# Optimization experiments

Hardware: AMD Instinct MI355X
Metric: run time of the kernel (lower is better)

Reference implementation:

```python
import jax, jax.numpy as jnp
import numpy as np

N_DRUG, N_CELL, N_GENE = 2048, 2048, 4096
N = N_DRUG + N_CELL + N_GENE
E = 262144
H1, H2, H3, HEADS = 256, 64, 64, 4
N_PAIRS = 10000
EPS = 1e-5


def _gatv2(x, src, dst, Wl, bl, Wr, br, att, bias, heads, out_ch):
    # PyG GATv2Conv: e_ij = att . leaky_relu(Wl x_j + Wr x_i), softmax over incoming edges of i,
    # out_i = sum_j alpha_ij * (Wl x_j), heads concatenated, plus output bias.
    n = x.shape[0]
    xl = (x @ Wl + bl).reshape(n, heads, out_ch)   # source transform
    xr = (x @ Wr + br).reshape(n, heads, out_ch)   # target transform
    e = jax.nn.leaky_relu(xl[src] + xr[dst], 0.2)  # [E, H, C]
    logits = jnp.einsum('ehc,hc->eh', e, att)      # [E, H]
    m = jax.ops.segment_max(logits, dst, num_segments=n)
    ex = jnp.exp(logits - m[dst])
    denom = jax.ops.segment_sum(ex, dst, num_segments=n)
    alpha = ex / denom[dst]                        # [E, H]
    out = jax.ops.segment_sum(xl[src] * alpha[:, :, None], dst, num_segments=n)
    return out.reshape(n, heads * out_ch) + bias, alpha


def _graph_norm(x, gamma, beta, mscale):
    # PyG GraphNorm over a single graph: out = (x - a*mean) / sqrt(var + eps) * gamma + beta
    mu = x.mean(0)
    sub = x - mu * mscale
    var = (sub * sub).mean(0)
    return sub / jnp.sqrt(var + EPS) * gamma + beta


def setup_inputs() -> dict:
    key = jax.random.key(0)
    ks = jax.random.split(key, 24)
    f = jnp.float32
    nrm = lambda k, shape, sc: jax.random.normal(k, shape, f) * sc
    drug = jax.random.normal(ks[0], (N_DRUG, N_DRUG), f)
    cell = jax.random.normal(ks[1], (N_CELL, N_CELL), f)
    gene = jax.random.normal(ks[2], (N_GENE, N_GENE), f)
    # random edges guaranteed to have no self loops (PyG would remove then re-add them)
    src = jax.random.randint(ks[3], (E,), 0, N)
    off = jax.random.randint(ks[4], (E,), 1, N)
    edges = jnp.stack([src, (src + off) % N]).astype(jnp.int32)
    idx_drug = jax.random.randint(ks[5], (N_PAIRS,), 0, N_DRUG)
    idx_cell = N_DRUG + jax.random.randint(ks[6], (N_PAIRS,), 0, N_CELL)
    HC2, HC3 = HEADS * H2, HEADS * H3
    return {
        'drug': drug, 'cell': cell, 'gene': gene,
        'edges': edges, 'idx_drug': idx_drug, 'idx_cell': idx_cell,
        'W_drug': nrm(ks[7], (N_DRUG, H1), 1 / np.sqrt(N_DRUG)), 'b_drug': jnp.zeros((H1,), f),
        'W_cell': nrm(ks[8], (N_CELL, H1), 1 / np.sqrt(N_CELL)), 'b_cell': jnp.zeros((H1,), f),
        'W_gene': nrm(ks[9], (N_GENE, H1), 1 / np.sqrt(N_GENE)), 'b_gene': jnp.zeros((H1,), f),
        'gat1_Wl': nrm(ks[10], (H1, HC2), 1 / np.sqrt(H1)), 'gat1_bl': jnp.zeros((HC2,), f),
        'gat1_Wr': nrm(ks[11], (H1, HC2), 1 / np.sqrt(H1)), 'gat1_br': jnp.zeros((HC2,), f),
        'gat1_att': nrm(ks[12], (HEADS, H2), 1 / np.sqrt(H2)), 'gat1_bias': jnp.zeros((HC2,), f),
        'gat2_Wl': nrm(ks[13], (HC2, HC3), 1 / np.sqrt(HC2)), 'gat2_bl': jnp.zeros((HC3,), f),
        'gat2_Wr': nrm(ks[14], (HC2, HC3), 1 / np.sqrt(HC2)), 'gat2_br': jnp.zeros((HC3,), f),
        'gat2_att': nrm(ks[15], (HEADS, H3), 1 / np.sqrt(H3)), 'gat2_bias': jnp.zeros((HC3,), f),
        'gn1_gamma': jnp.ones((HC2,), f), 'gn1_beta': jnp.zeros((HC2,), f), 'gn1_scale': jnp.ones((HC2,), f),
        'gn2_gamma': jnp.ones((HC3,), f), 'gn2_beta': jnp.zeros((HC3,), f), 'gn2_scale': jnp.ones((HC3,), f),
        'lin1_W': nrm(ks[16], (2 * HC3, 1), 1 / np.sqrt(2 * HC3)), 'lin1_b': jnp.zeros((1,), f),
    }


def reference(drug, cell, gene, edges, idx_drug, idx_cell,
              W_drug, b_drug, W_cell, b_cell, W_gene, b_gene,
              gat1_Wl, gat1_bl, gat1_Wr, gat1_br, gat1_att, gat1_bias,
              gat2_Wl, gat2_bl, gat2_Wr, gat2_br, gat2_att, gat2_bias,
              gn1_gamma, gn1_beta, gn1_scale, gn2_gamma, gn2_beta, gn2_scale,
              lin1_W, lin1_b):
    x = jnp.concatenate([drug @ W_drug + b_drug,
                         cell @ W_cell + b_cell,
                         gene @ W_gene + b_gene], axis=0)  # [N, H1]
    loops = jnp.arange(N, dtype=edges.dtype)
    src = jnp.concatenate([edges[0], loops])  # GATv2Conv adds self loops
    dst = jnp.concatenate([edges[1], loops])
    x, a1 = _gatv2(x, src, dst, gat1_Wl, gat1_bl, gat1_Wr, gat1_br, gat1_att, gat1_bias, HEADS, H2)
    x = jax.nn.relu(_graph_norm(x, gn1_gamma, gn1_beta, gn1_scale))  # dropout = identity (eval)
    x, a2 = _gatv2(x, src, dst, gat2_Wl, gat2_bl, gat2_Wr, gat2_br, gat2_att, gat2_bias, HEADS, H3)
    x = jax.nn.relu(_graph_norm(x, gn2_gamma, gn2_beta, gn2_scale))
    pair = jnp.concatenate([x[idx_drug], x[idx_cell]], axis=1)  # [P, 2*H*H3]
    pred = jax.nn.sigmoid(pair @ lin1_W + lin1_b)
    # get_attention_mat: dense [N,N], every edge position set to the (detached) scalar mean of
    # attention weights; the two layer matrices share edge positions so they simply add.
    val = jax.lax.stop_gradient(a1.mean() + a2.mean())
    attn = jnp.zeros((N, N), x.dtype).at[src, dst].set(val)
    return pred, attn
```

## Files before the change

### kernel.cpp

```cpp
#include <hip/hip_runtime.h>

#define NNODES 8192
#define NEDGE  262144
#define EETOT  270336
#define NPAIRS 10000

typedef __attribute__((ext_vector_type(8))) short s16x8;
typedef __attribute__((ext_vector_type(8))) unsigned short u16x8;
typedef __attribute__((ext_vector_type(4))) float f32x4;

__device__ __forceinline__ float lrelu(float v) { return v > 0.f ? v : 0.2f * v; }

__device__ __forceinline__ void split2(float a, unsigned short& h, unsigned short& l) {
  unsigned u = __float_as_uint(a);
  h = (unsigned short)(u >> 16);
  float hf = __uint_as_float(u & 0xffff0000u);
  float r = a - hf;
  unsigned v = __float_as_uint(r);
  v += 0x7fffu + ((v >> 16) & 1u);
  l = (unsigned short)(v >> 16);
}

__device__ __forceinline__ unsigned short f2bf(float f) {
  unsigned u = __float_as_uint(f);
  u += 0x7fffu + ((u >> 16) & 1u);
  return (unsigned short)(u >> 16);
}
__device__ __forceinline__ float bf2f(unsigned short u) {
  return __uint_as_float((unsigned)u << 16);
}

__device__ __forceinline__ void wsplit_body(const float* __restrict__ W,
    unsigned short* __restrict__ Th, int K, int blk) {
  int col = threadIdx.x;
  int kb = blk * 8;
  u16x8 vh;
#pragma unroll
  for (int i = 0; i < 8; ++i)
    vh[i] = f2bf(W[(size_t)(kb + i) * 256 + col]);
  *(u16x8*)(Th + (size_t)col * K + kb) = vh;
}

__global__ __launch_bounds__(256) void k_wsplit_all(
    const float* __restrict__ Wd, const float* __restrict__ Wc, const float* __restrict__ Wg,
    const float* __restrict__ W1l, const float* __restrict__ W1r,
    const float* __restrict__ W2l, const float* __restrict__ W2r,
    unsigned short* __restrict__ tdh, unsigned short* __restrict__ tch,
    unsigned short* __restrict__ tgh,
    unsigned short* __restrict__ tl1h, unsigned short* __restrict__ tr1h,
    unsigned short* __restrict__ tl2h, unsigned short* __restrict__ tr2h,
    int* __restrict__ counts_d, int* __restrict__ counts_s, float* __restrict__ stats) {
  int b = blockIdx.x;
  if      (b < 256)  wsplit_body(Wd,  tdh, 2048, b);
  else if (b < 512)  wsplit_body(Wc,  tch, 2048, b - 256);
  else if (b < 1024) wsplit_body(Wg,  tgh, 4096, b - 512);
  else if (b < 1056) { wsplit_body(W1l, tl1h, 256, b - 1024);
                       counts_d[(b - 1024) * 256 + threadIdx.x] = 0; }
  else if (b < 1088) { wsplit_body(W1r, tr1h, 256, b - 1056);
                       counts_s[(b - 1056) * 256 + threadIdx.x] = 0; }
  else if (b < 1120) { wsplit_body(W2l, tl2h, 256, b - 1088);
                       if (b < 1092) stats[(b - 1088) * 256 + threadIdx.x] = 0.f; }
  else               wsplit_body(W2r, tr2h, 256, b - 1120);
}

struct Tile128 {
  unsigned short Ah[128][40], Al[128][40], Bh[128][40];
};
struct TileN {
  Tile128 t;
  float nsc[256], nsh[256];
};

template<bool BIAS, bool OUTBF, bool NORM>
__device__ __forceinline__ void gemm_tile128(Tile128& s,
    const float* __restrict__ A, int lda,
    const unsigned short* __restrict__ Th, int ldb, int nsteps,
    const float* __restrict__ bias, float* __restrict__ C,
    unsigned short* __restrict__ Cb,
    const float* __restrict__ nsc, const float* __restrict__ nsh) {
  const int tid = threadIdx.x;
  const int wave = tid >> 6, lane = tid & 63;
  const int g = lane >> 4, r = lane & 15;
  const int wr = (wave >> 1) * 64, wc = (wave & 1) * 64;

  const int ar = tid >> 1, ak = (tid & 1) * 16;
  const float* Arow = A + (size_t)ar * lda + ak;
  const int bc = tid & 127, bk = (tid >> 7) * 16;
  const unsigned short* Bhs = Th + (size_t)bc * ldb + bk;

  f32x4 acc[4][4];
#pragma unroll
  for (int m = 0; m < 4; ++m)
#pragma unroll
    for (int n = 0; n < 4; ++n)
#pragma unroll
      for (int j = 0; j < 4; ++j) acc[m][n][j] = 0.f;

  float4 qa0 = *(const float4*)(Arow);
  float4 qa1 = *(const float4*)(Arow + 4);
  float4 qa2 = *(const float4*)(Arow + 8);
  float4 qa3 = *(const float4*)(Arow + 12);
  u16x8 qb0 = *(const u16x8*)(Bhs);
  u16x8 qb1 = *(const u16x8*)(Bhs + 8);
  float4 pa0, pa1, pa2, pa3;
  u16x8 pb0, pb1;
  if (nsteps > 1) {
    pa0 = *(const float4*)(Arow + 32);
    pa1 = *(const float4*)(Arow + 36);
    pa2 = *(const float4*)(Arow + 40);
    pa3 = *(const float4*)(Arow + 44);
    pb0 = *(const u16x8*)(Bhs + 32);
    pb1 = *(const u16x8*)(Bhs + 40);
  }

  for (int t = 0; t < nsteps; ++t) {
    {
      float av[16] = {qa0.x, qa0.y, qa0.z, qa0.w, qa1.x, qa1.y, qa1.z, qa1.w,
                      qa2.x, qa2.y, qa2.z, qa2.w, qa3.x, qa3.y, qa3.z, qa3.w};
      u16x8 vh0, vh1, vl0, vl1;
#pragma unroll
      for (int i = 0; i < 16; ++i) {
        float v = av[i];
        if constexpr (NORM) {
          int ch = t * 32 + ak + i;
          v = fmaxf(v * nsc[ch] + nsh[ch], 0.f);
        }
        unsigned short hh, ll;
        split2(v, hh, ll);
        if (i < 8) { vh0[i] = hh; vl0[i] = ll; }
        else       { vh1[i - 8] = hh; vl1[i - 8] = ll; }
      }
      *(u16x8*)&s.Ah[ar][ak]     = vh0;
      *(u16x8*)&s.Ah[ar][ak + 8] = vh1;
      *(u16x8*)&s.Al[ar][ak]     = vl0;
      *(u16x8*)&s.Al[ar][ak + 8] = vl1;
      *(u16x8*)&s.Bh[bc][bk]     = qb0;
      *(u16x8*)&s.Bh[bc][bk + 8] = qb1;
    }
    __syncthreads();
    qa0 = pa0; qa1 = pa1; qa2 = pa2; qa3 = pa3;
    qb0 = pb0; qb1 = pb1;
    if (t + 2 < nsteps) {
      const float* An = Arow + (size_t)(t + 2) * 32;
      pa0 = *(const float4*)(An);
      pa1 = *(const float4*)(An + 4);
      pa2 = *(const float4*)(An + 8);
      pa3 = *(const float4*)(An + 12);
      const unsigned short* Bhn = Bhs + (size_t)(t + 2) * 32;
      pb0 = *(const u16x8*)(Bhn);
      pb1 = *(const u16x8*)(Bhn + 8);
    }
    s16x8 fah[4], fal[4], fbh[4];
#pragma unroll
    for (int m = 0; m < 4; ++m) {
      fah[m] = *(const s16x8*)&s.Ah[wr + m * 16 + r][g * 8];
      fal[m] = *(const s16x8*)&s.Al[wr + m * 16 + r][g * 8];
    }
#pragma unroll
    for (int n = 0; n < 4; ++n)
      fbh[n] = *(const s16x8*)&s.Bh[wc + n * 16 + r][g * 8];
#pragma unroll
    for (int m = 0; m < 4; ++m)
#pragma unroll
      for (int n = 0; n < 4; ++n) {
        acc[m][n] = __builtin_amdgcn_mfma_f32_16x16x32_bf16(fal[m], fbh[n], acc[m][n], 0, 0, 0);
        acc[m][n] = __builtin_amdgcn_mfma_f32_16x16x32_bf16(fah[m], fbh[n], acc[m][n], 0, 0, 0);
      }
    __syncthreads();
  }
#pragma unroll
  for (int m = 0; m < 4; ++m)
#pragma unroll
    for (int n = 0; n < 4; ++n) {
      int col = wc + n * 16 + r;
      float bv = BIAS ? bias[col] : 0.f;
      int rowb = wr + m * 16 + g * 4;
#pragma unroll
      for (int j = 0; j < 4; ++j) {
        float v = acc[m][n][j] + bv;
        if constexpr (OUTBF) Cb[(size_t)(rowb + j) * 256 + col] = f2bf(v);
        else                 C[(size_t)(rowb + j) * 256 + col] = v;
      }
    }
}

#define PDRUG_PLANE ((size_t)2048 * 256)
#define PGENE_PLANE ((size_t)4096 * 256)
__global__ __launch_bounds__(256) void k_inproj_fill(
    const float* __restrict__ drug, const float* __restrict__ cell,
    const float* __restrict__ gene,
    const unsigned short* __restrict__ tdh, const unsigned short* __restrict__ tch,
    const unsigned short* __restrict__ tgh, float* __restrict__ P,
    const int* __restrict__ csrdst, const int* __restrict__ rowst_s,
    float* __restrict__ attn) {
  __shared__ Tile128 s;
  int b = blockIdx.x;
  if (b >= 512) {
    int row = b - 512;
    float* rp = attn + (size_t)row * NNODES;
    f32x4* p4 = (f32x4*)rp;
    f32x4 z = {0.f, 0.f, 0.f, 0.f};
#pragma unroll
    for (int j = 0; j < 8; ++j)
      __builtin_nontemporal_store(z, p4 + j * 256 + threadIdx.x);
    __syncthreads();
    int e0 = rowst_s[row], e1 = rowst_s[row + 1];
    for (int j = e0 + (int)threadIdx.x; j < e1; j += 256)
      rp[csrdst[j]] = 16384.0f / 270336.0f;
    return;
  }
  if (b < 256) {
    int idx = b & 127;
    int colblk = (idx >> 3) & 1;
    int rest = (idx & 7) | ((idx >> 4) << 3);
    int rowblk = rest >> 2, chunk = rest & 3;
    const float* X = (b < 128) ? drug : cell;
    const unsigned short* Th = (b < 128) ? tdh : tch;
    float* Pb = P + ((b < 128) ? 0 : 4 * PDRUG_PLANE);
    gemm_tile128<false, false, false>(s,
        X + (size_t)rowblk * 128 * 2048 + (size_t)chunk * 512, 2048,
        Th + (size_t)colblk * 128 * 2048 + chunk * 512, 2048, 16, nullptr,
        Pb + (size_t)chunk * PDRUG_PLANE + (size_t)rowblk * 128 * 256 + colblk * 128,
        nullptr, nullptr, nullptr);
  } else {
    int idx = b - 256;
    int colblk = (idx >> 3) & 1;
    int rest = (idx & 7) | ((idx >> 4) << 3);
    int rowblk = rest >> 2, chunk = rest & 3;
    gemm_tile128<false, false, false>(s,
        gene + (size_t)rowblk * 128 * 4096 + (size_t)chunk * 1024, 4096,
        tgh + (size_t)colblk * 128 * 4096 + chunk * 1024, 4096, 32, nullptr,
        P + 8 * PDRUG_PLANE + (size_t)chunk * PGENE_PLANE + (size_t)rowblk * 128 * 256 + colblk * 128,
        nullptr, nullptr, nullptr);
  }
}

__global__ __launch_bounds__(256) void k_reduce(const float* __restrict__ P,
    const float* __restrict__ bd, const float* __restrict__ bc,
    const float* __restrict__ bg, float* __restrict__ out) {
  int idx = blockIdx.x * 256 + threadIdx.x;
  size_t e = (size_t)idx * 4;
  int row = (int)(e >> 8);
  int col = (int)(e & 255);
  const float* base; const float* bias; size_t plane;
  if (row < 2048) {
    base = P + (size_t)row * 256 + col; bias = bd; plane = PDRUG_PLANE;
  } else if (row < 4096) {
    base = P + 4 * PDRUG_PLANE + (size_t)(row - 2048) * 256 + col; bias = bc;
    plane = PDRUG_PLANE;
  } else {
    base = P + 8 * PDRUG_PLANE + (size_t)(row - 4096) * 256 + col; bias = bg;
    plane = PGENE_PLANE;
  }
  float4 s = *(const float4*)(base);
#pragma unroll
  for (int p = 1; p < 4; ++p) {
    float4 v = *(const float4*)(base + p * plane);
    s.x += v.x; s.y += v.y; s.z += v.z; s.w += v.w;
  }
  float4 bv = *(const float4*)(bias + col);
  s.x += bv.x; s.y += bv.y; s.z += bv.z; s.w += bv.w;
  *(float4*)(out + e) = s;
}

template<bool NORM>
__global__ __launch_bounds__(256) void k_gemm2(const float* __restrict__ A,
    const unsigned short* __restrict__ ThL, const unsigned short* __restrict__ ThR,
    const float* __restrict__ biasL, const float* __restrict__ biasR,
    unsigned short* __restrict__ CLb, unsigned short* __restrict__ CRb,
    const float* __restrict__ csum, const float* __restrict__ csumsq,
    const float* __restrict__ gamma, const float* __restrict__ beta,
    const float* __restrict__ mscale) {
  __shared__ TileN s;
  int b = blockIdx.x;
  int sub = (b >> 3) & 3;
  int x = (b & 7) | ((b >> 5) << 3);
  if constexpr (NORM) {
    int c = threadIdx.x;
    float mu = csum[c] * (1.0f / 8192.0f);
    float ex2 = csumsq[c] * (1.0f / 8192.0f);
    float smu = mscale[c] * mu;
    float var = ex2 - 2.f * smu * mu + smu * smu;
    float sc = rsqrtf(var + 1e-5f) * gamma[c];
    s.nsc[c] = sc;
    s.nsh[c] = beta[c] - smu * sc;
    __syncthreads();
  }
  int row0 = x * 128;
  int col0 = (sub & 1) * 128;
  if (sub >= 2) {
    gemm_tile128<true, true, NORM>(s.t, A + (size_t)row0 * 256, 256,
        ThR + (size_t)col0 * 256, 256, 8,
        biasR + col0, nullptr, CRb + (size_t)row0 * 256 + col0, s.nsc, s.nsh);
  } else {
    gemm_tile128<true, true, NORM>(s.t, A + (size_t)row0 * 256, 256,
        ThL + (size_t)col0 * 256, 256, 8,
        biasL + col0, nullptr, CLb + (size_t)row0 * 256 + col0, s.nsc, s.nsh);
  }
}

__global__ void k_count2(const int* __restrict__ edges, int* __restrict__ cd,
                         int* __restrict__ cs) {
  int e = blockIdx.x * blockDim.x + threadIdx.x;
  if (e >= EETOT) return;
  int s, d;
  if (e < NEDGE) { s = edges[e]; d = edges[NEDGE + e]; } else { s = d = e - NEDGE; }
  atomicAdd(&cd[d], 1);
  atomicAdd(&cs[s], 1);
}

__global__ __launch_bounds__(1024) void k_scan2(
    const int* __restrict__ c0, int* __restrict__ r0, int* __restrict__ u0,
    const int* __restrict__ c1, int* __restrict__ r1, int* __restrict__ u1) {
  const int* counts = blockIdx.x ? c1 : c0;
  int* row_start = blockIdx.x ? r1 : r0;
  int* cursor = blockIdx.x ? u1 : u0;
  __shared__ int part[1024];
  int t = threadIdx.x;
  int base = t * 8;
  int loc[8];
  int s = 0;
#pragma unroll
  for (int j = 0; j < 8; ++j) { loc[j] = s; s += counts[base + j]; }
  part[t] = s;
  __syncthreads();
  for (int off = 1; off < 1024; off <<= 1) {
    int v = (t >= off) ? part[t - off] : 0;
    __syncthreads();
    part[t] += v;
    __syncthreads();
  }
  int pre = (t == 0) ? 0 : part[t - 1];
#pragma unroll
  for (int j = 0; j < 8; ++j) {
    int v = pre + loc[j];
    row_start[base + j] = v;
    cursor[base + j] = v;
  }
  if (t == 1023) row_start[NNODES] = pre + s;
}

__global__ void k_place2(const int* __restrict__ edges, int* __restrict__ curd,
    int* __restrict__ curs, int* __restrict__ csrsrc, int* __restrict__ csrdst) {
  int e = blockIdx.x * blockDim.x + threadIdx.x;
  if (e >= EETOT) return;
  int s, d;
  if (e < NEDGE) { s = edges[e]; d = edges[NEDGE + e]; } else { s = d = e - NEDGE; }
  int pd = atomicAdd(&curd[d], 1);
  csrsrc[pd] = s;
  int ps = atomicAdd(&curs[s], 1);
  csrdst[ps] = d;
}

__global__ __launch_bounds__(256) void k_gat(
    const unsigned short* __restrict__ xl, const unsigned short* __restrict__ xr,
    const float* __restrict__ att, const int* __restrict__ csrsrc,
    const int* __restrict__ row_start, const float* __restrict__ bias,
    float* __restrict__ out) {
  int i = blockIdx.x * 4 + (threadIdx.x >> 6);
  int lane = threadIdx.x & 63;
  int co = (lane >> 4) * 64 + (lane & 15) * 4;
  float4 w4 = *(const float4*)(att + co);
  ushort4 ur = *(const ushort4*)(xr + (size_t)i * 256 + co);
  float4 r4;
  r4.x = bf2f(ur.x); r4.y = bf2f(ur.y); r4.z = bf2f(ur.z); r4.w = bf2f(ur.w);
  float sum = 0.f, ax = 0.f, ay = 0.f, az = 0.f, aw = 0.f;
  int e0 = row_start[i], e1 = row_start[i + 1];
  int deg = e1 - e0;

  for (int cb = 0; cb < deg; cb += 64) {
    int cn = min(deg - cb, 64);
    int myid = (lane < cn) ? csrsrc[e0 + cb + lane] : 0;
    auto g = [&](int j) {
      int s = __shfl(myid, j);
      return *(const ushort4*)(xl + (size_t)s * 256 + co);
    };
    ushort4 cur[8], nxt[8];
    int curn = min(cn, 8);
#pragma unroll
    for (int j = 0; j < 8; ++j)
      if (j < curn) cur[j] = g(j);
    int p = curn;
    for (;;) {
      int nxtn = min(cn - p, 8);
#pragma unroll
      for (int j = 0; j < 8; ++j)
        if (j < nxtn) nxt[j] = g(p + j);
#pragma unroll
      for (int j = 0; j < 8; ++j) {
        if (j >= curn) break;
        ushort4 u = cur[j];
        float x0 = bf2f(u.x), x1 = bf2f(u.y), x2 = bf2f(u.z), x3 = bf2f(u.w);
        float t = w4.x * lrelu(x0 + r4.x) + w4.y * lrelu(x1 + r4.y) +
                  w4.z * lrelu(x2 + r4.z) + w4.w * lrelu(x3 + r4.w);
        t += __shfl_xor(t, 1);
        t += __shfl_xor(t, 2);
        t += __shfl_xor(t, 4);
        t += __shfl_xor(t, 8);
        float el = __expf(fminf(t, 60.f));
        sum += el;
        ax += el * x0; ay += el * x1; az += el * x2; aw += el * x3;
      }
      if (nxtn <= 0) break;
#pragma unroll
      for (int j = 0; j < 8; ++j) cur[j] = nxt[j];
      curn = nxtn; p += nxtn;
    }
  }
  float inv = 1.0f / sum;
  float4 bv = *(const float4*)(bias + co);
  float4 r;
  r.x = ax * inv + bv.x; r.y = ay * inv + bv.y;
  r.z = az * inv + bv.z; r.w = aw * inv + bv.w;
  *(float4*)(out + (size_t)i * 256 + co) = r;
}

__global__ __launch_bounds__(256) void k_colstats(const float* __restrict__ x,
    float* __restrict__ csum, float* __restrict__ csumsq) {
  int c = threadIdx.x;
  int r0 = blockIdx.x * 32;
  float s = 0.f, s2 = 0.f;
  for (int r = 0; r < 32; ++r) {
    float v = x[(size_t)(r0 + r) * 256 + c];
    s += v; s2 += v * v;
  }
  atomicAdd(&csum[c], s);
  atomicAdd(&csumsq[c], s2);
}

__global__ __launch_bounds__(256) void k_pred(const float* __restrict__ h,
    const int* __restrict__ idx_drug, const int* __restrict__ idx_cell,
    const float* __restrict__ W, const float* __restrict__ b,
    const float* __restrict__ csum, const float* __restrict__ csumsq,
    const float* __restrict__ gamma, const float* __restrict__ beta,
    const float* __restrict__ mscale, float* __restrict__ out) {
  int p = blockIdx.x * 4 + (threadIdx.x >> 6);
  if (p >= NPAIRS) return;
  int lane = threadIdx.x & 63;
  int rd = idx_drug[p], rc = idx_cell[p];
  float4 a  = *(const float4*)(h + (size_t)rd * 256 + lane * 4);
  float4 cg = *(const float4*)(h + (size_t)rc * 256 + lane * 4);
  float4 wa = *(const float4*)(W + lane * 4);
  float4 wc = *(const float4*)(W + 256 + lane * 4);
  float av[4] = {a.x, a.y, a.z, a.w};
  float cv[4] = {cg.x, cg.y, cg.z, cg.w};
  float wv[4] = {wa.x, wa.y, wa.z, wa.w};
  float uv[4] = {wc.x, wc.y, wc.z, wc.w};
  float t = 0.f;
#pragma unroll
  for (int j = 0; j < 4; ++j) {
    int ch = lane * 4 + j;
    float mu = csum[ch] * (1.0f / 8192.0f);
    float ex2 = csumsq[ch] * (1.0f / 8192.0f);
    float smu = mscale[ch] * mu;
    float var = ex2 - 2.f * smu * mu + smu * smu;
    float sc = rsqrtf(var + 1e-5f) * gamma[ch];
    float sh = beta[ch] - smu * sc;
    t += fmaxf(av[j] * sc + sh, 0.f) * wv[j] + fmaxf(cv[j] * sc + sh, 0.f) * uv[j];
  }
#pragma unroll
  for (int off = 1; off < 64; off <<= 1) t += __shfl_xor(t, off);
  if (lane == 0) out[p] = 1.0f / (1.0f + __expf(-(t + b[0])));
}

extern "C" void kernel_launch(void* const* d_in, const int* in_sizes, int n_in,
                              void* d_out, int out_size, void* d_ws, size_t ws_size,
                              hipStream_t stream) {
  const float* drug = (const float*)d_in[0];
  const float* cell = (const float*)d_in[1];
  const float* gene = (const float*)d_in[2];
  const int*   edges = (const int*)d_in[3];
  const int*   idxd = (const int*)d_in[4];
  const int*   idxc = (const int*)d_in[5];
  const float* Wd = (const float*)d_in[6];   const float* bd = (const float*)d_in[7];
  const float* Wc = (const float*)d_in[8];   const float* bc = (const float*)d_in[9];
  const float* Wg = (const float*)d_in[10];  const float* bg = (const float*)d_in[11];
  const float* g1Wl = (const float*)d_in[12]; const float* g1bl = (const float*)d_in[13];
  const float* g1Wr = (const float*)d_in[14]; const float* g1br = (const float*)d_in[15];
  const float* g1att = (const float*)d_in[16]; const float* g1bias = (const float*)d_in[17];
  const float* g2Wl = (const float*)d_in[18]; const float* g2bl = (const float*)d_in[19];
  const float* g2Wr = (const float*)d_in[20]; const float* g2br = (const float*)d_in[21];
  const float* g2att = (const float*)d_in[22]; const float* g2bias = (const float*)d_in[23];
  const float* gn1g = (const float*)d_in[24]; const float* gn1b = (const float*)d_in[25];
  const float* gn1s = (const float*)d_in[26];
  const float* gn2g = (const float*)d_in[27]; const float* gn2b = (const float*)d_in[28];
  const float* gn2s = (const float*)d_in[29];
  const float* linW = (const float*)d_in[30]; const float* linb = (const float*)d_in[31];
  float* out = (float*)d_out;
  (void)in_sizes; (void)n_in; (void)out_size; (void)ws_size;

  char* ws = (char*)d_ws;
  size_t off = 0;
  auto take = [&](size_t bytes) -> void* {
    void* p = ws + off;
    off += (bytes + 255) & ~(size_t)255;
    return p;
  };
  float* bufA = (float*)take((size_t)NNODES * 256 * 4);
  unsigned short* bufBb = (unsigned short*)take((size_t)NNODES * 256 * 2);
  unsigned short* bufCb = (unsigned short*)take((size_t)NNODES * 256 * 2);
  int* counts_d = (int*)take((size_t)NNODES * 4);
  int* counts_s = (int*)take((size_t)NNODES * 4);
  float* stats  = (float*)take(4 * 256 * 4);
  int* rowst_d  = (int*)take((size_t)(NNODES + 1) * 4);
  int* rowst_s  = (int*)take((size_t)(NNODES + 1) * 4);
  int* cursor_d = (int*)take((size_t)NNODES * 4);
  int* cursor_s = (int*)take((size_t)NNODES * 4);
  int* csrsrc   = (int*)take((size_t)EETOT * 4);
  int* csrdst   = (int*)take((size_t)EETOT * 4);
  unsigned short* tdh = (unsigned short*)take((size_t)256 * 2048 * 2);
  unsigned short* tch = (unsigned short*)take((size_t)256 * 2048 * 2);
  unsigned short* tgh = (unsigned short*)take((size_t)256 * 4096 * 2);
  unsigned short* tl1h = (unsigned short*)take((size_t)256 * 256 * 2);
  unsigned short* tr1h = (unsigned short*)take((size_t)256 * 256 * 2);
  unsigned short* tl2h = (unsigned short*)take((size_t)256 * 256 * 2);
  unsigned short* tr2h = (unsigned short*)take((size_t)256 * 256 * 2);
  float* Ppart = (float*)take((8 * PDRUG_PLANE + 4 * PGENE_PLANE) * 4);

  k_wsplit_all<<<1152, 256, 0, stream>>>(Wd, Wc, Wg, g1Wl, g1Wr, g2Wl, g2Wr,
      tdh, tch, tgh, tl1h, tr1h, tl2h, tr2h, counts_d, counts_s, stats);

  k_count2<<<EETOT / 256, 256, 0, stream>>>(edges, counts_d, counts_s);
  k_scan2<<<2, 1024, 0, stream>>>(counts_d, rowst_d, cursor_d, counts_s, rowst_s, cursor_s);
  k_place2<<<EETOT / 256, 256, 0, stream>>>(edges, cursor_d, cursor_s, csrsrc, csrdst);

  k_inproj_fill<<<512 + NNODES, 256, 0, stream>>>(drug, cell, gene, tdh, tch, tgh,
      Ppart, csrdst, rowst_s, out + NPAIRS);
  k_reduce<<<NNODES * 256 / 4 / 256, 256, 0, stream>>>(Ppart, bd, bc, bg, bufA);

  k_gemm2<false><<<256, 256, 0, stream>>>(bufA, tl1h, tr1h, g1bl, g1br,
      bufBb, bufCb, nullptr, nullptr, nullptr, nullptr, nullptr);
  k_gat<<<NNODES / 4, 256, 0, stream>>>(bufBb, bufCb, g1att, csrsrc, rowst_d, g1bias, bufA);
  k_colstats<<<NNODES / 32, 256, 0, stream>>>(bufA, stats, stats + 256);

  k_gemm2<true><<<256, 256, 0, stream>>>(bufA, tl2h, tr2h, g2bl, g2br,
      bufBb, bufCb, stats, stats + 256, gn1g, gn1b, gn1s);
  k_gat<<<NNODES / 4, 256, 0, stream>>>(bufBb, bufCb, g2att, csrsrc, rowst_d, g2bias, bufA);
  k_colstats<<<NNODES / 32, 256, 0, stream>>>(bufA, stats + 512, stats + 768);

  k_pred<<<NPAIRS / 4, 256, 0, stream>>>(bufA, idxd, idxc, linW, linb,
      stats + 512, stats + 768, gn2g, gn2b, gn2s, out);
}
```

Before: 291.1 us.

## Spread dense attention-matrix fill across GEMM and GAT kernels

The 8192x8192 attention matrix fill (zeroing plus edge scatter) used to run entirely as extra blocks of the input-projection kernel. It is now split into 1024-row slices appended as extra blocks to the input projection, both small GEMMs and both GAT kernels. The goal is to overlap this bandwidth-bound work with compute- and latency-bound phases that underuse the GPU. The cost is extra parameters and a branch in each kernel, and the fill blocks may compete with the main blocks for memory bandwidth.

```diff
diff --git a/kernel.cpp b/kernel.cpp
--- a/kernel.cpp
+++ b/kernel.cpp
@@ -28,6 +28,20 @@
 }
 __device__ __forceinline__ float bf2f(unsigned short u) {
   return __uint_as_float((unsigned)u << 16);
+}
+
+__device__ __forceinline__ void attn_fill_row(int row, const int* __restrict__ csrdst,
+    const int* __restrict__ rowst_s, float* __restrict__ attn) {
+  float* rp = attn + (size_t)row * NNODES;
+  f32x4* p4 = (f32x4*)rp;
+  f32x4 z = {0.f, 0.f, 0.f, 0.f};
+#pragma unroll
+  for (int j = 0; j < 8; ++j)
+    __builtin_nontemporal_store(z, p4 + j * 256 + threadIdx.x);
+  __syncthreads();
+  int e0 = rowst_s[row], e1 = rowst_s[row + 1];
+  for (int j = e0 + (int)threadIdx.x; j < e1; j += 256)
+    rp[csrdst[j]] = 16384.0f / 270336.0f;
 }
 
 __device__ __forceinline__ void wsplit_body(const float* __restrict__ W,
@@ -195,20 +209,7 @@
     float* __restrict__ attn) {
   __shared__ Tile128 s;
   int b = blockIdx.x;
-  if (b >= 512) {
-    int row = b - 512;
-    float* rp = attn + (size_t)row * NNODES;
-    f32x4* p4 = (f32x4*)rp;
-    f32x4 z = {0.f, 0.f, 0.f, 0.f};
-#pragma unroll
-    for (int j = 0; j < 8; ++j)
-      __builtin_nontemporal_store(z, p4 + j * 256 + threadIdx.x);
-    __syncthreads();
-    int e0 = rowst_s[row], e1 = rowst_s[row + 1];
-    for (int j = e0 + (int)threadIdx.x; j < e1; j += 256)
-      rp[csrdst[j]] = 16384.0f / 270336.0f;
-    return;
-  }
+  if (b >= 512) { attn_fill_row(b - 512, csrdst, rowst_s, attn); return; }
   if (b < 256) {
     int idx = b & 127;
     int colblk = (idx >> 3) & 1;
@@ -270,9 +271,12 @@
     unsigned short* __restrict__ CLb, unsigned short* __restrict__ CRb,
     const float* __restrict__ csum, const float* __restrict__ csumsq,
     const float* __restrict__ gamma, const float* __restrict__ beta,
-    const float* __restrict__ mscale) {
+    const float* __restrict__ mscale,
+    const int* __restrict__ csrdst, const int* __restrict__ rowst_s,
+    float* __restrict__ attn, int fill_base) {
   __shared__ TileN s;
   int b = blockIdx.x;
+  if (b >= 256) { attn_fill_row(fill_base + b - 256, csrdst, rowst_s, attn); return; }
   int sub = (b >> 3) & 3;
   int x = (b & 7) | ((b >> 5) << 3);
   if constexpr (NORM) {
@@ -356,7 +360,13 @@
     const unsigned short* __restrict__ xl, const unsigned short* __restrict__ xr,
     const float* __restrict__ att, const int* __restrict__ csrsrc,
     const int* __restrict__ row_start, const float* __restrict__ bias,
-    float* __restrict__ out) {
+    float* __restrict__ out,
+    const int* __restrict__ csrdst, const int* __restrict__ rowst_s,
+    float* __restrict__ attn, int fill_base) {
+  if (blockIdx.x >= 2048) {
+    attn_fill_row(fill_base + blockIdx.x - 2048, csrdst, rowst_s, attn);
+    return;
+  }
   int i = blockIdx.x * 4 + (threadIdx.x >> 6);
   int lane = threadIdx.x & 63;
   int co = (lane >> 4) * 64 + (lane & 15) * 4;
@@ -516,6 +526,7 @@
   unsigned short* tl2h = (unsigned short*)take((size_t)256 * 256 * 2);
   unsigned short* tr2h = (unsigned short*)take((size_t)256 * 256 * 2);
   float* Ppart = (float*)take((8 * PDRUG_PLANE + 4 * PGENE_PLANE) * 4);
+  float* attn = out + NPAIRS;
 
   k_wsplit_all<<<1152, 256, 0, stream>>>(Wd, Wc, Wg, g1Wl, g1Wr, g2Wl, g2Wr,
       tdh, tch, tgh, tl1h, tr1h, tl2h, tr2h, counts_d, counts_s, stats);
@@ -524,18 +535,22 @@
   k_scan2<<<2, 1024, 0, stream>>>(counts_d, rowst_d, cursor_d, counts_s, rowst_s, cursor_s);
   k_place2<<<EETOT / 256, 256, 0, stream>>>(edges, cursor_d, cursor_s, csrsrc, csrdst);
 
-  k_inproj_fill<<<512 + NNODES, 256, 0, stream>>>(drug, cell, gene, tdh, tch, tgh,
-      Ppart, csrdst, rowst_s, out + NPAIRS);
+  k_inproj_fill<<<512 + 4096, 256, 0, stream>>>(drug, cell, gene, tdh, tch, tgh,
+      Ppart, csrdst, rowst_s, attn);
   k_reduce<<<NNODES * 256 / 4 / 256, 256, 0, stream>>>(Ppart, bd, bc, bg, bufA);
 
-  k_gemm2<false><<<256, 256, 0, stream>>>(bufA, tl1h, tr1h, g1bl, g1br,
-      bufBb, bufCb, nullptr, nullptr, nullptr, nullptr, nullptr);
-  k_gat<<<NNODES / 4, 256, 0, stream>>>(bufBb, bufCb, g1att, csrsrc, rowst_d, g1bias, bufA);
+  k_gemm2<false><<<256 + 1024, 256, 0, stream>>>(bufA, tl1h, tr1h, g1bl, g1br,
+      bufBb, bufCb, nullptr, nullptr, nullptr, nullptr, nullptr,
+      csrdst, rowst_s, attn, 4096);
+  k_gat<<<2048 + 1024, 256, 0, stream>>>(bufBb, bufCb, g1att, csrsrc, rowst_d, g1bias,
+      bufA, csrdst, rowst_s, attn, 5120);
   k_colstats<<<NNODES / 32, 256, 0, stream>>>(bufA, stats, stats + 256);
 
-  k_gemm2<true><<<256, 256, 0, stream>>>(bufA, tl2h, tr2h, g2bl, g2br,
-      bufBb, bufCb, stats, stats + 256, gn1g, gn1b, gn1s);
-  k_gat<<<NNODES / 4, 256, 0, stream>>>(bufBb, bufCb, g2att, csrsrc, rowst_d, g2bias, bufA);
+  k_gemm2<true><<<256 + 1024, 256, 0, stream>>>(bufA, tl2h, tr2h, g2bl, g2br,
+      bufBb, bufCb, stats, stats + 256, gn1g, gn1b, gn1s,
+      csrdst, rowst_s, attn, 6144);
+  k_gat<<<2048 + 1024, 256, 0, stream>>>(bufBb, bufCb, g2att, csrsrc, rowst_d, g2bias,
+      bufA, csrdst, rowst_s, attn, 7168);
   k_colstats<<<NNODES / 32, 256, 0, stream>>>(bufA, stats + 512, stats + 768);
 
   k_pred<<<NPAIRS / 4, 256, 0, stream>>>(bufA, idxd, idxc, linW, linb,
```

Result: faster. 280.9 us, median of 2 (-3.5%).
